# Kernel optimization log

Measured on AMD Instinct MI355X. Metric: run time of the kernel, lower is better.

The kernel has to match this reference:

```python
import jax, jax.numpy as jnp
import numpy as np

H_OUT = 2
H_DIM = 256
V_DIM = 128
Q_DIM = 128


def setup_inputs() -> dict:
    key = jax.random.key(0)
    ks = jax.random.split(key, 10)
    B, NV, NQ = 8, 128, 512
    s = 0.02
    return {
        "v": jax.random.normal(ks[0], (B, NV, V_DIM), dtype=jnp.float32),
        "q": jax.random.normal(ks[1], (B, NQ, Q_DIM), dtype=jnp.float32),
        "Wv": jax.random.normal(ks[2], (V_DIM, H_DIM * H_OUT), dtype=jnp.float32) * s,
        "bv": jax.random.normal(ks[3], (H_DIM * H_OUT,), dtype=jnp.float32) * s,
        "Wq": jax.random.normal(ks[4], (Q_DIM, H_DIM * H_OUT), dtype=jnp.float32) * s,
        "bq": jax.random.normal(ks[5], (H_DIM * H_OUT,), dtype=jnp.float32) * s,
        "wa": jax.random.normal(ks[6], (H_DIM,), dtype=jnp.float32) * s,
        "ba": jax.random.normal(ks[7], (), dtype=jnp.float32) * s,
        "Wo": jax.random.normal(ks[8], (H_OUT * H_DIM, H_DIM), dtype=jnp.float32) * s,
        "bo": jax.random.normal(ks[9], (H_DIM,), dtype=jnp.float32) * s,
    }


def reference(v, q, Wv, bv, Wq, bq, wa, ba, Wo, bo):
    B, NV, _ = v.shape
    NQ = q.shape[1]
    # projections -> (B, N, h_out, h_dim)
    v_ = (v @ Wv + bv).reshape(B, NV, H_OUT, H_DIM)
    q_ = (q @ Wq + bq).reshape(B, NQ, H_OUT, H_DIM)
    # att_proj on the outer product, without materializing the joint tensor:
    # score[b,h,i,j] = sum_d v_[b,i,h,d]*q_[b,j,h,d]*wa[d] + ba
    score = jnp.einsum("bihd,bjhd,d->bhij", v_, q_, wa) + ba
    att = jax.nn.softmax(score, axis=2)  # softmax over num_v (dim=2), as in torch
    # weighted sum: head[b,h,d] = sum_{i,j} att[b,h,i,j]*v_[b,i,h,d]*q_[b,j,h,d]
    ctx = jnp.einsum("bhij,bjhd->bihd", att, q_)
    head = jnp.einsum("bihd,bihd->bhd", ctx, v_)
    fused = head.reshape(B, H_OUT * H_DIM) @ Wo + bo
    att_out = att.reshape(B, H_OUT, NV * NQ, 1)  # matches torch's final view+unsqueeze
    return fused, att_out
```

## Files before the change

kernel.cpp:

```cpp
#include <hip/hip_runtime.h>
#include <math.h>

#define B_  8
#define NV_ 128
#define NQ_ 512
#define KD_ 128
#define P_  512
#define H_  2
#define D_  256

typedef unsigned short ushort_t;
typedef unsigned int   uint_t;
typedef __attribute__((ext_vector_type(8))) short bf16x8;
typedef __attribute__((ext_vector_type(4))) float f32x4;

#define QBF_OFF  0
#define VWA_OFF  (4u<<20)
#define VT_OFF   (5u<<20)
#define HEAD_OFF (6u<<20)

__device__ __forceinline__ ushort_t f2b(float f) {
    uint_t u = __float_as_uint(f);
    uint_t r = (u + 0x7FFFu + ((u >> 16) & 1u)) >> 16;
    return (ushort_t)r;
}
__device__ __forceinline__ float b2f(ushort_t u) {
    return __uint_as_float(((uint_t)u) << 16);
}

extern "C" __global__ void __launch_bounds__(256) proj_kernel(
    const float* __restrict__ v, const float* __restrict__ q,
    const float* __restrict__ Wv, const float* __restrict__ bv,
    const float* __restrict__ Wq, const float* __restrict__ bq,
    const float* __restrict__ wa, char* __restrict__ ws)
{
    ushort_t* qbf  = (ushort_t*)(ws + QBF_OFF);
    ushort_t* vwa  = (ushort_t*)(ws + VWA_OFF);
    ushort_t* vT   = (ushort_t*)(ws + VT_OFF);
    float*    head = (float*)(ws + HEAD_OFF);

    __shared__ __align__(16) float ls[16 * KD_];

    const int bid = blockIdx.x, t = threadIdx.x;
    const bool is_v = (bid < 64);
    const float* src; const float* W; const float* bias;
    int rb;
    if (is_v) { rb = bid * 16;        src = v + (size_t)rb * KD_; W = Wv; bias = bv; }
    else      { rb = (bid - 64) * 16; src = q + (size_t)rb * KD_; W = Wq; bias = bq; }

    if (bid < 16) head[bid * 256 + t] = 0.f;

    for (int idx = t; idx < 16 * KD_; idx += 256) ls[idx] = src[idx];
    __syncthreads();

    const int c0 = t, c1 = t + 256;
    float acc0[16], acc1[16];
#pragma unroll
    for (int r = 0; r < 16; ++r) { acc0[r] = 0.f; acc1[r] = 0.f; }

    for (int k = 0; k < KD_; k += 4) {
        const float w00 = W[(size_t)(k+0)*P_ + c0], w01 = W[(size_t)(k+1)*P_ + c0];
        const float w02 = W[(size_t)(k+2)*P_ + c0], w03 = W[(size_t)(k+3)*P_ + c0];
        const float w10 = W[(size_t)(k+0)*P_ + c1], w11 = W[(size_t)(k+1)*P_ + c1];
        const float w12 = W[(size_t)(k+2)*P_ + c1], w13 = W[(size_t)(k+3)*P_ + c1];
#pragma unroll
        for (int r = 0; r < 16; ++r) {
            const float4 a = *(const float4*)&ls[r * KD_ + k];
            acc0[r] = fmaf(a.w, w03, fmaf(a.z, w02, fmaf(a.y, w01, fmaf(a.x, w00, acc0[r]))));
            acc1[r] = fmaf(a.w, w13, fmaf(a.z, w12, fmaf(a.y, w11, fmaf(a.x, w10, acc1[r]))));
        }
    }
    const float b0 = bias[c0], b1 = bias[c1];
    const float wa_t = wa[t];

    if (is_v) {
        const int b  = rb >> 7;
        const int i0 = rb & 127;
        const size_t bh0 = (size_t)(b * 2 + 0), bh1 = (size_t)(b * 2 + 1);
#pragma unroll
        for (int r = 0; r < 16; ++r) {
            const int i = i0 + r;
            const float v0 = acc0[r] + b0, v1 = acc1[r] + b1;
            vwa[(bh0 * 128 + i) * 256 + t] = f2b(v0 * wa_t);
            vwa[(bh1 * 128 + i) * 256 + t] = f2b(v1 * wa_t);
            vT [(bh0 * 256 + t) * 128 + i] = f2b(v0);
            vT [(bh1 * 256 + t) * 128 + i] = f2b(v1);
        }
    } else {
        const int b  = rb >> 9;
        const int j0q = rb & 511;
        const size_t bh0 = (size_t)(b * 2 + 0), bh1 = (size_t)(b * 2 + 1);
#pragma unroll
        for (int r = 0; r < 16; ++r) {
            const int j = j0q + r;
            qbf[(bh0 * 512 + j) * 256 + t] = f2b(acc0[r] + b0);
            qbf[(bh1 * 512 + j) * 256 + t] = f2b(acc1[r] + b1);
        }
    }
}

extern "C" __global__ void __launch_bounds__(256) att_kernel(
    char* __restrict__ ws, float* __restrict__ out)
{
    const ushort_t* qbf = (const ushort_t*)(ws + QBF_OFF);
    const ushort_t* vwa = (const ushort_t*)(ws + VWA_OFF);
    const ushort_t* vT  = (const ushort_t*)(ws + VT_OFF);
    float*          head = (float*)(ws + HEAD_OFF);
    float*          att_out = out + B_ * D_;

    __shared__ ushort_t q_lds[32][264];
    __shared__ ushort_t p_lds[32][136];
    __shared__ float wmax[4][32];
    __shared__ float wsum[4][32];

    const int t  = threadIdx.x;
    const int w  = t >> 6;
    const int l  = t & 63;
    const int l15 = l & 15, lg = l >> 4;

    const int bid = blockIdx.x;
    const int jt  = bid & 15;
    const int h   = (bid >> 4) & 1;
    const int b   = bid >> 5;
    const int j0  = jt * 32;
    const size_t bh = (size_t)(b * H_ + h);

    const ushort_t* vwa_p = vwa + bh * 128 * 256;
    const ushort_t* vT_p  = vT  + bh * 256 * 128;
    const ushort_t* qp    = qbf + (bh * 512 + j0) * 256;

    for (int c = t; c < 1024; c += 256) {
        const int row = c >> 5, c8 = (c & 31) * 8;
        *(bf16x8*)&q_lds[row][c8] = *(const bf16x8*)&qp[(size_t)row * 256 + c8];
    }
    __syncthreads();

    const ushort_t* a0 = vwa_p + (size_t)(w * 32 + l15) * 256 + lg * 8;
    const ushort_t* a1 = a0 + 16 * 256;
    const ushort_t* bq0 = &q_lds[l15][lg * 8];
    const ushort_t* bq1 = &q_lds[l15 + 16][lg * 8];

    f32x4 acc[2][2];
#pragma unroll
    for (int mb = 0; mb < 2; ++mb)
#pragma unroll
        for (int nb = 0; nb < 2; ++nb) acc[mb][nb] = (f32x4){0.f, 0.f, 0.f, 0.f};

#pragma unroll
    for (int ks = 0; ks < 8; ++ks) {
        const int ko = ks * 32;
        const bf16x8 A0 = *(const bf16x8*)(a0 + ko);
        const bf16x8 A1 = *(const bf16x8*)(a1 + ko);
        const bf16x8 B0 = *(const bf16x8*)(bq0 + ko);
        const bf16x8 B1 = *(const bf16x8*)(bq1 + ko);
        acc[0][0] = __builtin_amdgcn_mfma_f32_16x16x32_bf16(A0, B0, acc[0][0], 0, 0, 0);
        acc[0][1] = __builtin_amdgcn_mfma_f32_16x16x32_bf16(A0, B1, acc[0][1], 0, 0, 0);
        acc[1][0] = __builtin_amdgcn_mfma_f32_16x16x32_bf16(A1, B0, acc[1][0], 0, 0, 0);
        acc[1][1] = __builtin_amdgcn_mfma_f32_16x16x32_bf16(A1, B1, acc[1][1], 0, 0, 0);
    }

    float mx[2];
#pragma unroll
    for (int nb = 0; nb < 2; ++nb) {
        float m = acc[0][nb][0];
#pragma unroll
        for (int mb = 0; mb < 2; ++mb)
#pragma unroll
            for (int r = 0; r < 4; ++r) m = fmaxf(m, acc[mb][nb][r]);
        m = fmaxf(m, __shfl_xor(m, 16));
        m = fmaxf(m, __shfl_xor(m, 32));
        mx[nb] = m;
    }
    if (l < 16) { wmax[w][l] = mx[0]; wmax[w][l + 16] = mx[1]; }
    __syncthreads();

    float cm[2];
#pragma unroll
    for (int nb = 0; nb < 2; ++nb) {
        const int jl = nb * 16 + l15;
        cm[nb] = fmaxf(fmaxf(wmax[0][jl], wmax[1][jl]), fmaxf(wmax[2][jl], wmax[3][jl]));
    }

    float sm[2] = {0.f, 0.f};
#pragma unroll
    for (int mb = 0; mb < 2; ++mb)
#pragma unroll
        for (int nb = 0; nb < 2; ++nb)
#pragma unroll
            for (int r = 0; r < 4; ++r) {
                const float e = __expf(acc[mb][nb][r] - cm[nb]);
                acc[mb][nb][r] = e;
                sm[nb] += e;
            }
#pragma unroll
    for (int nb = 0; nb < 2; ++nb) {
        sm[nb] += __shfl_xor(sm[nb], 16);
        sm[nb] += __shfl_xor(sm[nb], 32);
    }
    if (l < 16) { wsum[w][l] = sm[0]; wsum[w][l + 16] = sm[1]; }
    __syncthreads();

    float cinv[2];
#pragma unroll
    for (int nb = 0; nb < 2; ++nb) {
        const int jl = nb * 16 + l15;
        cinv[nb] = 1.f / (wsum[0][jl] + wsum[1][jl] + wsum[2][jl] + wsum[3][jl]);
    }

    float* attp = att_out + (bh * 128) * 512 + j0;
#pragma unroll
    for (int mb = 0; mb < 2; ++mb) {
        const int il = w * 32 + mb * 16 + lg * 4;
#pragma unroll
        for (int nb = 0; nb < 2; ++nb) {
            const int jl = nb * 16 + l15;
            float p0 = acc[mb][nb][0] * cinv[nb];
            float p1 = acc[mb][nb][1] * cinv[nb];
            float p2 = acc[mb][nb][2] * cinv[nb];
            float p3 = acc[mb][nb][3] * cinv[nb];
            attp[(size_t)(il + 0) * 512 + jl] = p0;
            attp[(size_t)(il + 1) * 512 + jl] = p1;
            attp[(size_t)(il + 2) * 512 + jl] = p2;
            attp[(size_t)(il + 3) * 512 + jl] = p3;
            const uint_t u01 = (uint_t)f2b(p0) | ((uint_t)f2b(p1) << 16);
            const uint_t u23 = (uint_t)f2b(p2) | ((uint_t)f2b(p3) << 16);
            *(uint_t*)&p_lds[jl][il + 0] = u01;
            *(uint_t*)&p_lds[jl][il + 2] = u23;
        }
    }
    __syncthreads();

    f32x4 wacc[2][4];
#pragma unroll
    for (int mb = 0; mb < 2; ++mb)
#pragma unroll
        for (int nb = 0; nb < 4; ++nb) wacc[mb][nb] = (f32x4){0.f, 0.f, 0.f, 0.f};

    const ushort_t* pb0 = &p_lds[l15][lg * 8];
    const ushort_t* pb1 = &p_lds[l15 + 16][lg * 8];
    const ushort_t* vb0 = vT_p + (size_t)(w * 64 +  0 + l15) * 128 + lg * 8;
    const ushort_t* vb1 = vT_p + (size_t)(w * 64 + 16 + l15) * 128 + lg * 8;
    const ushort_t* vb2 = vT_p + (size_t)(w * 64 + 32 + l15) * 128 + lg * 8;
    const ushort_t* vb3 = vT_p + (size_t)(w * 64 + 48 + l15) * 128 + lg * 8;

#pragma unroll
    for (int ks = 0; ks < 4; ++ks) {
        const int ko = ks * 32;
        const bf16x8 PA0 = *(const bf16x8*)(pb0 + ko);
        const bf16x8 PA1 = *(const bf16x8*)(pb1 + ko);
        const bf16x8 VB0 = *(const bf16x8*)(vb0 + ko);
        const bf16x8 VB1 = *(const bf16x8*)(vb1 + ko);
        const bf16x8 VB2 = *(const bf16x8*)(vb2 + ko);
        const bf16x8 VB3 = *(const bf16x8*)(vb3 + ko);
        wacc[0][0] = __builtin_amdgcn_mfma_f32_16x16x32_bf16(PA0, VB0, wacc[0][0], 0, 0, 0);
        wacc[1][0] = __builtin_amdgcn_mfma_f32_16x16x32_bf16(PA1, VB0, wacc[1][0], 0, 0, 0);
        wacc[0][1] = __builtin_amdgcn_mfma_f32_16x16x32_bf16(PA0, VB1, wacc[0][1], 0, 0, 0);
        wacc[1][1] = __builtin_amdgcn_mfma_f32_16x16x32_bf16(PA1, VB1, wacc[1][1], 0, 0, 0);
        wacc[0][2] = __builtin_amdgcn_mfma_f32_16x16x32_bf16(PA0, VB2, wacc[0][2], 0, 0, 0);
        wacc[1][2] = __builtin_amdgcn_mfma_f32_16x16x32_bf16(PA1, VB2, wacc[1][2], 0, 0, 0);
        wacc[0][3] = __builtin_amdgcn_mfma_f32_16x16x32_bf16(PA0, VB3, wacc[0][3], 0, 0, 0);
        wacc[1][3] = __builtin_amdgcn_mfma_f32_16x16x32_bf16(PA1, VB3, wacc[1][3], 0, 0, 0);
    }

    float hd[4] = {0.f, 0.f, 0.f, 0.f};
#pragma unroll
    for (int nb = 0; nb < 4; ++nb) {
        const int d = w * 64 + nb * 16 + l15;
#pragma unroll
        for (int mb = 0; mb < 2; ++mb)
#pragma unroll
            for (int r = 0; r < 4; ++r) {
                const int jl = mb * 16 + lg * 4 + r;
                hd[nb] = fmaf(wacc[mb][nb][r], b2f(q_lds[jl][d]), hd[nb]);
            }
        hd[nb] += __shfl_xor(hd[nb], 16);
        hd[nb] += __shfl_xor(hd[nb], 32);
    }
    if (l < 16) {
        float* hp = head + bh * 256 + w * 64 + l;
        atomicAdd(hp +  0, hd[0]);
        atomicAdd(hp + 16, hd[1]);
        atomicAdd(hp + 32, hd[2]);
        atomicAdd(hp + 48, hd[3]);
    }
}

extern "C" __global__ void __launch_bounds__(256) out_kernel(
    const float* __restrict__ Wo, const float* __restrict__ bo,
    const char* __restrict__ ws, float* __restrict__ out)
{
    const float* head = (const float*)(ws + HEAD_OFF);
    __shared__ __align__(16) float hs[512];
    __shared__ float ored[4][64];

    const int bid = blockIdx.x, t = threadIdx.x;
    const int b = bid >> 2, cg = bid & 3;
    const int col = cg * 64 + (t & 63), kq = t >> 6;

    hs[t]       = head[(size_t)b * 512 + t];
    hs[t + 256] = head[(size_t)b * 512 + t + 256];
    __syncthreads();

    float acc = 0.f;
    const int kbeg = kq * 128;
    for (int k = kbeg; k < kbeg + 128; k += 4) {
        const float4 hk = *(const float4*)&hs[k];
        acc = fmaf(hk.x, Wo[(size_t)(k+0)*256 + col], acc);
        acc = fmaf(hk.y, Wo[(size_t)(k+1)*256 + col], acc);
        acc = fmaf(hk.z, Wo[(size_t)(k+2)*256 + col], acc);
        acc = fmaf(hk.w, Wo[(size_t)(k+3)*256 + col], acc);
    }
    ored[kq][t & 63] = acc;
    __syncthreads();
    if (t < 64) {
        const float r = ored[0][t] + ored[1][t] + ored[2][t] + ored[3][t] + bo[col];
        out[(size_t)b * 256 + col] = r;
    }
}

extern "C" void kernel_launch(void* const* d_in, const int* in_sizes, int n_in,
                              void* d_out, int out_size, void* d_ws, size_t ws_size,
                              hipStream_t stream)
{
    const float* v  = (const float*)d_in[0];
    const float* q  = (const float*)d_in[1];
    const float* Wv = (const float*)d_in[2];
    const float* bv = (const float*)d_in[3];
    const float* Wq = (const float*)d_in[4];
    const float* bq = (const float*)d_in[5];
    const float* wa = (const float*)d_in[6];
    const float* Wo = (const float*)d_in[8];
    const float* bo = (const float*)d_in[9];
    float* out = (float*)d_out;
    char*  ws  = (char*)d_ws;

    hipLaunchKernelGGL(proj_kernel, dim3(320), dim3(256), 0, stream,
                       v, q, Wv, bv, Wq, bq, wa, ws);
    hipLaunchKernelGGL(att_kernel,  dim3(256), dim3(256), 0, stream, ws, out);
    hipLaunchKernelGGL(out_kernel,  dim3(32),  dim3(256), 0, stream, Wo, bo, ws, out);
}
```

Before: 112.7 us.

## Move projection GEMM to bf16 MFMA with pre-transposed bf16 weights

Adds a prep kernel that converts Wv and Wq to bf16 and transposes them into workspace, and also zeroes the head accumulator. The projection kernel is rewritten to run 64-row tiles on bf16 MFMA instructions instead of scalar fp32 FMAs. Results are staged through LDS so qbf, vwa and vT can be written as coalesced 16-byte stores. The aim is to cut the compute and uncoalesced-store cost of the projections, at the price of an extra kernel launch, fewer blocks (80), and rounding the inputs to bf16 before the matmul, which costs some precision.

```diff
diff --git a/kernel.cpp b/kernel.cpp
--- a/kernel.cpp
+++ b/kernel.cpp
@@ -17,7 +17,9 @@
 #define QBF_OFF  0
 #define VWA_OFF  (4u<<20)
 #define VT_OFF   (5u<<20)
-#define HEAD_OFF (6u<<20)
+#define HEAD_OFF (7u<<20)
+#define WVT_OFF  (8u<<20)
+#define WQT_OFF  ((8u<<20) + (128u<<10))
 
 __device__ __forceinline__ ushort_t f2b(float f) {
     uint_t u = __float_as_uint(f);
@@ -28,74 +30,151 @@
     return __uint_as_float(((uint_t)u) << 16);
 }
 
-extern "C" __global__ void __launch_bounds__(256) proj_kernel(
+extern "C" __global__ void __launch_bounds__(256) prep_kernel(
+    const float* __restrict__ Wv, const float* __restrict__ Wq,
+    char* __restrict__ ws)
+{
+    ushort_t* wvt = (ushort_t*)(ws + WVT_OFF);
+    ushort_t* wqt = (ushort_t*)(ws + WQT_OFF);
+    float*    head = (float*)(ws + HEAD_OFF);
+
+    __shared__ ushort_t lt[128][132];
+
+    const int bid = blockIdx.x, t = threadIdx.x;
+    const int wsel = bid >> 2, cc = bid & 3, c0 = cc * 128;
+    const float* W = wsel ? Wq : Wv;
+    ushort_t*   WT = wsel ? wqt : wvt;
+
+    head[bid * 512 + t] = 0.f;
+    head[bid * 512 + t + 256] = 0.f;
+
+    for (int it = 0; it < 16; ++it) {
+        const int idx = it * 256 + t;
+        const int k = idx >> 5, cq = (idx & 31) * 4;
+        const float4 f = *(const float4*)&W[(size_t)k * P_ + c0 + cq];
+        uint_t* dst = (uint_t*)&lt[k][cq];
+        dst[0] = (uint_t)f2b(f.x) | ((uint_t)f2b(f.y) << 16);
+        dst[1] = (uint_t)f2b(f.z) | ((uint_t)f2b(f.w) << 16);
+    }
+    __syncthreads();
+
+    for (int it = 0; it < 8; ++it) {
+        const int idx = it * 256 + t;
+        const int c = idx & 127, kg = idx >> 7;
+        bf16x8 u;
+#pragma unroll
+        for (int r = 0; r < 8; ++r) u[r] = (short)lt[kg * 8 + r][c];
+        *(bf16x8*)&WT[(size_t)(c0 + c) * 128 + kg * 8] = u;
+    }
+}
+
+extern "C" __global__ void __launch_bounds__(256, 1) proj_kernel(
     const float* __restrict__ v, const float* __restrict__ q,
-    const float* __restrict__ Wv, const float* __restrict__ bv,
-    const float* __restrict__ Wq, const float* __restrict__ bq,
+    const float* __restrict__ bv, const float* __restrict__ bq,
     const float* __restrict__ wa, char* __restrict__ ws)
 {
-    ushort_t* qbf  = (ushort_t*)(ws + QBF_OFF);
-    ushort_t* vwa  = (ushort_t*)(ws + VWA_OFF);
-    ushort_t* vT   = (ushort_t*)(ws + VT_OFF);
-    float*    head = (float*)(ws + HEAD_OFF);
-
-    __shared__ __align__(16) float ls[16 * KD_];
+    ushort_t* qbf = (ushort_t*)(ws + QBF_OFF);
+    ushort_t* vwa = (ushort_t*)(ws + VWA_OFF);
+    ushort_t* vT  = (ushort_t*)(ws + VT_OFF);
+
+    __shared__ __align__(16) char ldsb[64 * 264 * 2];
+    ushort_t (*A)[136] = (ushort_t (*)[136])ldsb;
+    ushort_t (*O)[264] = (ushort_t (*)[264])ldsb;
 
     const int bid = blockIdx.x, t = threadIdx.x;
-    const bool is_v = (bid < 64);
-    const float* src; const float* W; const float* bias;
-    int rb;
-    if (is_v) { rb = bid * 16;        src = v + (size_t)rb * KD_; W = Wv; bias = bv; }
-    else      { rb = (bid - 64) * 16; src = q + (size_t)rb * KD_; W = Wq; bias = bq; }
-
-    if (bid < 16) head[bid * 256 + t] = 0.f;
-
-    for (int idx = t; idx < 16 * KD_; idx += 256) ls[idx] = src[idx];
-    __syncthreads();
-
-    const int c0 = t, c1 = t + 256;
-    float acc0[16], acc1[16];
-#pragma unroll
-    for (int r = 0; r < 16; ++r) { acc0[r] = 0.f; acc1[r] = 0.f; }
-
-    for (int k = 0; k < KD_; k += 4) {
-        const float w00 = W[(size_t)(k+0)*P_ + c0], w01 = W[(size_t)(k+1)*P_ + c0];
-        const float w02 = W[(size_t)(k+2)*P_ + c0], w03 = W[(size_t)(k+3)*P_ + c0];
-        const float w10 = W[(size_t)(k+0)*P_ + c1], w11 = W[(size_t)(k+1)*P_ + c1];
-        const float w12 = W[(size_t)(k+2)*P_ + c1], w13 = W[(size_t)(k+3)*P_ + c1];
-#pragma unroll
-        for (int r = 0; r < 16; ++r) {
-            const float4 a = *(const float4*)&ls[r * KD_ + k];
-            acc0[r] = fmaf(a.w, w03, fmaf(a.z, w02, fmaf(a.y, w01, fmaf(a.x, w00, acc0[r]))));
-            acc1[r] = fmaf(a.w, w13, fmaf(a.z, w12, fmaf(a.y, w11, fmaf(a.x, w10, acc1[r]))));
+    const int w = t >> 6, l = t & 63, l15 = l & 15, lg = l >> 4;
+
+    const bool is_v = (bid < 16);
+    int b, r0;
+    const float* src; const float* bias;
+    if (is_v) { const int tv = bid;      b = tv >> 1; r0 = (tv & 1) * 64; src = v + (size_t)(b * NV_ + r0) * KD_; bias = bv; }
+    else      { const int tq = bid - 16; b = tq >> 3; r0 = (tq & 7) * 64; src = q + (size_t)(b * NQ_ + r0) * KD_; bias = bq; }
+    const ushort_t* WT = (const ushort_t*)(ws + (is_v ? WVT_OFF : WQT_OFF));
+
+    for (int it = 0; it < 8; ++it) {
+        const int idx = it * 256 + t;
+        const int row = idx >> 5, kq = (idx & 31) * 4;
+        const float4 f = *(const float4*)&src[(size_t)row * KD_ + kq];
+        uint_t* dst = (uint_t*)&A[row][kq];
+        dst[0] = (uint_t)f2b(f.x) | ((uint_t)f2b(f.y) << 16);
+        dst[1] = (uint_t)f2b(f.z) | ((uint_t)f2b(f.w) << 16);
+    }
+    __syncthreads();
+
+    const int n0 = w * 128;
+    f32x4 acc[4][8];
+#pragma unroll
+    for (int mf = 0; mf < 4; ++mf)
+#pragma unroll
+        for (int nf = 0; nf < 8; ++nf) acc[mf][nf] = (f32x4){0.f, 0.f, 0.f, 0.f};
+
+#pragma unroll
+    for (int ks = 0; ks < 4; ++ks) {
+        const int ko = ks * 32 + lg * 8;
+        bf16x8 Af[4];
+#pragma unroll
+        for (int mf = 0; mf < 4; ++mf)
+            Af[mf] = *(const bf16x8*)&A[mf * 16 + l15][ko];
+        bf16x8 Bf[8];
+#pragma unroll
+        for (int nf = 0; nf < 8; ++nf)
+            Bf[nf] = *(const bf16x8*)&WT[(size_t)(n0 + nf * 16 + l15) * 128 + ko];
+#pragma unroll
+        for (int mf = 0; mf < 4; ++mf)
+#pragma unroll
+            for (int nf = 0; nf < 8; ++nf)
+                acc[mf][nf] = __builtin_amdgcn_mfma_f32_16x16x32_bf16(Af[mf], Bf[nf], acc[mf][nf], 0, 0, 0);
+    }
+    __syncthreads();
+
+    for (int p = 0; p < 2; ++p) {
+        if ((w >> 1) == p) {
+            const int nbase = (w & 1) * 128;
+#pragma unroll
+            for (int mf = 0; mf < 4; ++mf)
+#pragma unroll
+                for (int nf = 0; nf < 8; ++nf) {
+                    const int m = mf * 16 + lg * 4;
+                    const int n = nbase + nf * 16 + l15;
+                    const float bcol = bias[p * 256 + n];
+#pragma unroll
+                    for (int r = 0; r < 4; ++r)
+                        O[m + r][n] = f2b(acc[mf][nf][r] + bcol);
+                }
         }
-    }
-    const float b0 = bias[c0], b1 = bias[c1];
-    const float wa_t = wa[t];
-
-    if (is_v) {
-        const int b  = rb >> 7;
-        const int i0 = rb & 127;
-        const size_t bh0 = (size_t)(b * 2 + 0), bh1 = (size_t)(b * 2 + 1);
-#pragma unroll
-        for (int r = 0; r < 16; ++r) {
-            const int i = i0 + r;
-            const float v0 = acc0[r] + b0, v1 = acc1[r] + b1;
-            vwa[(bh0 * 128 + i) * 256 + t] = f2b(v0 * wa_t);
-            vwa[(bh1 * 128 + i) * 256 + t] = f2b(v1 * wa_t);
-            vT [(bh0 * 256 + t) * 128 + i] = f2b(v0);
-            vT [(bh1 * 256 + t) * 128 + i] = f2b(v1);
+        __syncthreads();
+        for (int it = 0; it < 8; ++it) {
+            const int idx = it * 256 + t;
+            const int row = idx >> 5, d0 = (idx & 31) * 8;
+            const bf16x8 u = *(const bf16x8*)&O[row][d0];
+            if (is_v) {
+                const float4 wa0 = *(const float4*)&wa[d0];
+                const float4 wa1 = *(const float4*)&wa[d0 + 4];
+                bf16x8 s;
+                s[0] = (short)f2b(b2f((ushort_t)u[0]) * wa0.x);
+                s[1] = (short)f2b(b2f((ushort_t)u[1]) * wa0.y);
+                s[2] = (short)f2b(b2f((ushort_t)u[2]) * wa0.z);
+                s[3] = (short)f2b(b2f((ushort_t)u[3]) * wa0.w);
+                s[4] = (short)f2b(b2f((ushort_t)u[4]) * wa1.x);
+                s[5] = (short)f2b(b2f((ushort_t)u[5]) * wa1.y);
+                s[6] = (short)f2b(b2f((ushort_t)u[6]) * wa1.z);
+                s[7] = (short)f2b(b2f((ushort_t)u[7]) * wa1.w);
+                *(bf16x8*)&vwa[((size_t)(b * 2 + p) * 128 + r0 + row) * 256 + d0] = s;
+            } else {
+                *(bf16x8*)&qbf[((size_t)(b * 2 + p) * 512 + r0 + row) * 256 + d0] = u;
+            }
         }
-    } else {
-        const int b  = rb >> 9;
-        const int j0q = rb & 511;
-        const size_t bh0 = (size_t)(b * 2 + 0), bh1 = (size_t)(b * 2 + 1);
-#pragma unroll
-        for (int r = 0; r < 16; ++r) {
-            const int j = j0q + r;
-            qbf[(bh0 * 512 + j) * 256 + t] = f2b(acc0[r] + b0);
-            qbf[(bh1 * 512 + j) * 256 + t] = f2b(acc1[r] + b1);
+        if (is_v) {
+            for (int it = 0; it < 8; ++it) {
+                const int d  = (t & 63) + (it & 3) * 64;
+                const int ic = (t >> 6) + (it >> 2) * 4;
+                bf16x8 u;
+#pragma unroll
+                for (int r = 0; r < 8; ++r) u[r] = (short)O[ic * 8 + r][d];
+                *(bf16x8*)&vT[((size_t)(b * 2 + p) * 256 + d) * 128 + r0 + ic * 8] = u;
+            }
         }
+        __syncthreads();
     }
 }
 
@@ -334,8 +413,8 @@
     float* out = (float*)d_out;
     char*  ws  = (char*)d_ws;
 
-    hipLaunchKernelGGL(proj_kernel, dim3(320), dim3(256), 0, stream,
-                       v, q, Wv, bv, Wq, bq, wa, ws);
+    hipLaunchKernelGGL(prep_kernel, dim3(8),   dim3(256), 0, stream, Wv, Wq, ws);
+    hipLaunchKernelGGL(proj_kernel, dim3(80),  dim3(256), 0, stream, v, q, bv, bq, wa, ws);
     hipLaunchKernelGGL(att_kernel,  dim3(256), dim3(256), 0, stream, ws, out);
     hipLaunchKernelGGL(out_kernel,  dim3(32),  dim3(256), 0, stream, Wo, bo, ws, out);
 }
```

Result: faster. 106.1 us (-5.8%).
